# Kernel optimization log

Measured on AMD Instinct MI355X. Metric: run time of the kernel, lower is better.

Reference implementation:

```python
import jax, jax.numpy as jnp
import numpy as np

N = 50000   # nodes
E = 800000  # edges
F = 128     # node_features
H = 128     # hid_channel
G = 128     # graphs in batch


def _lin(k, din, dout):
    s = 1.0 / np.sqrt(din)
    return jax.random.uniform(k, (din, dout), jnp.float32, -s, s)


def setup_inputs() -> dict:
    key = jax.random.key(0)
    ks = jax.random.split(key, 16)
    x = jax.random.normal(ks[0], (N, F), jnp.float32)
    edge_list = jax.random.randint(ks[1], (E, 2), 0, N)
    batch = jnp.sort(jax.random.randint(ks[2], (N,), 0, G))
    inp = {"x": x, "edge_list": edge_list, "batch": batch}
    dims = [(F, H)] + [(H, H)] * 4
    for i, (di, do) in enumerate(dims):
        k1, k2 = jax.random.split(ks[3 + i])
        inp[f"Wl{i+1}"] = _lin(k1, di, do)   # weight on aggregated neighbors
        inp[f"Wr{i+1}"] = _lin(k2, di, do)   # root (self) weight
        inp[f"b{i+1}"] = jnp.zeros((do,), jnp.float32)
    inp["Wf1"] = _lin(ks[10], H, H)
    inp["bf1"] = jnp.zeros((H,), jnp.float32)
    inp["Wf2"] = _lin(ks[11], H, 1)
    inp["bf2"] = jnp.zeros((1,), jnp.float32)
    return inp


def reference(x, edge_list, batch,
              Wl1, Wr1, b1, Wl2, Wr2, b2, Wl3, Wr3, b3,
              Wl4, Wr4, b4, Wl5, Wr5, b5, Wf1, bf1, Wf2, bf2):
    src = edge_list[:, 0]  # message source (x_j)
    dst = edge_list[:, 1]  # aggregation target
    ones_e = jnp.ones((E,), x.dtype)
    deg = jnp.clip(jax.ops.segment_sum(ones_e, dst, num_segments=N), 1.0)

    def sage(h, Wl, Wr, b):
        # scatter-mean of neighbor features, then two linears (PyG SAGEConv, aggr='mean')
        agg = jax.ops.segment_sum(h[src], dst, num_segments=N) / deg[:, None]
        return agg @ Wl + h @ Wr + b

    h = x
    for Wl, Wr, b in ((Wl1, Wr1, b1), (Wl2, Wr2, b2), (Wl3, Wr3, b3),
                      (Wl4, Wr4, b4), (Wl5, Wr5, b5)):
        h = jax.nn.relu(sage(h, Wl, Wr, b))

    # global mean pool over graphs
    cnt = jnp.clip(jax.ops.segment_sum(jnp.ones((N,), h.dtype), batch, num_segments=G), 1.0)
    g = jax.ops.segment_sum(h, batch, num_segments=G) / cnt[:, None]

    g = jax.nn.relu(g @ Wf1 + bf1)
    out = jax.nn.sigmoid(g @ Wf2 + bf2)  # num_classes==1 binary path
    return out.reshape(-1)
```

## Files before the change

### kernel.cpp

```cpp
#include <hip/hip_runtime.h>
#include <math.h>

#define N_NODES 50000
#define MPAD    50048
#define N_EDGES 800000
#define FDIM    128
#define NGRAPH  128

#define NCB   196
#define CBN   256
#define ABLK  256
#define EPB   (N_EDGES / ABLK)
#define CVT_BLOCKS ((MPAD * FDIM / 4 + 255) / 256)

#define NCHUNK 8
#define CHUNK_OF(s) ((int)(((u32)(s) * 671u) >> 22))

typedef __attribute__((ext_vector_type(8))) short short8;
typedef __attribute__((ext_vector_type(4))) float f32x4;
typedef __attribute__((ext_vector_type(2))) float f32x2;
typedef unsigned int u32;

__device__ __forceinline__ unsigned short f2bf(float f) {
    unsigned int u = __float_as_uint(f);
    return (unsigned short)((u + 0x7FFFu + ((u >> 16) & 1u)) >> 16);
}
__device__ __forceinline__ float bfhi(unsigned int u) { return __uint_as_float(u & 0xFFFF0000u); }
__device__ __forceinline__ float bflo(unsigned int u) { return __uint_as_float(u << 16); }

#define ACC16(v) { \
    f32x2 d0 = __builtin_amdgcn_cvt_pk_f32_fp8((int)(v).x, false); \
    f32x2 d1 = __builtin_amdgcn_cvt_pk_f32_fp8((int)(v).x, true);  \
    f32x2 d2 = __builtin_amdgcn_cvt_pk_f32_fp8((int)(v).y, false); \
    f32x2 d3 = __builtin_amdgcn_cvt_pk_f32_fp8((int)(v).y, true);  \
    f32x2 d4 = __builtin_amdgcn_cvt_pk_f32_fp8((int)(v).z, false); \
    f32x2 d5 = __builtin_amdgcn_cvt_pk_f32_fp8((int)(v).z, true);  \
    f32x2 d6 = __builtin_amdgcn_cvt_pk_f32_fp8((int)(v).w, false); \
    f32x2 d7 = __builtin_amdgcn_cvt_pk_f32_fp8((int)(v).w, true);  \
    acc[0] += d0.x;  acc[1] += d0.y;  acc[2] += d1.x;  acc[3] += d1.y; \
    acc[4] += d2.x;  acc[5] += d2.y;  acc[6] += d3.x;  acc[7] += d3.y; \
    acc[8] += d4.x;  acc[9] += d4.y;  acc[10] += d5.x; acc[11] += d5.y; \
    acc[12] += d6.x; acc[13] += d6.y; acc[14] += d7.x; acc[15] += d7.y; }

__global__ __launch_bounds__(256) void pre_kernel(const float* __restrict__ x,
                                                  unsigned short* __restrict__ xb,
                                                  unsigned char* __restrict__ xb8,
                                                  const int* __restrict__ edges,
                                                  int* __restrict__ g_hist) {
    __shared__ int hist[NCB];
    int t = threadIdx.x;
    if (blockIdx.x < CVT_BLOCKS) {
        int i = blockIdx.x * 256 + t;
        if (i >= MPAD * FDIM / 4) return;
        int base = i * 4;
        uint2 o;
        if (base < N_NODES * FDIM) {
            float4 v = *(const float4*)&x[base];
            o.x = (u32)f2bf(v.x) | ((u32)f2bf(v.y) << 16);
            o.y = (u32)f2bf(v.z) | ((u32)f2bf(v.w) << 16);
            int p8 = __builtin_amdgcn_cvt_pk_fp8_f32(v.x, v.y, 0, false);
            p8 = __builtin_amdgcn_cvt_pk_fp8_f32(v.z, v.w, p8, true);
            *(u32*)&xb8[base] = (u32)p8;
        } else { o.x = 0u; o.y = 0u; }
        *(uint2*)&xb[base] = o;
    } else {
        int blk = blockIdx.x - CVT_BLOCKS;
        if (t < NCB) hist[t] = 0;
        __syncthreads();
        int beg = blk * EPB, end = beg + EPB;
        for (int i = beg + t; i < end; i += 256) {
            int2 ed = ((const int2*)edges)[i];
            atomicAdd(&hist[ed.y >> 8], 1);
        }
        __syncthreads();
        if (t < NCB) g_hist[t * ABLK + blk] = hist[t];
    }
}

__global__ __launch_bounds__(64) void scan1_kernel(const int* __restrict__ g_hist,
                                                   int* __restrict__ g_base,
                                                   int* __restrict__ cbtotal) {
    int cbi = blockIdx.x, l = threadIdx.x;
    int4 v = ((const int4*)(g_hist + cbi * ABLK))[l];
    int s1 = v.x + v.y, s2 = s1 + v.z, s3 = s2 + v.w;
    int inc = s3;
    #pragma unroll
    for (int off = 1; off < 64; off <<= 1) {
        int nv = __shfl_up(inc, off, 64);
        if (l >= off) inc += nv;
    }
    int excl = inc - s3;
    int4 o; o.x = excl; o.y = excl + v.x; o.z = excl + s1; o.w = excl + s2;
    ((int4*)(g_base + cbi * ABLK))[l] = o;
    if (l == 63) cbtotal[cbi] = inc;
}

__global__ __launch_bounds__(256) void scan2_kernel(const int* __restrict__ cbtotal,
                                                    int* __restrict__ cbbase,
                                                    int* __restrict__ row_ptr) {
    __shared__ int s[NCB];
    int t = threadIdx.x;
    if (t < NCB) s[t] = cbtotal[t];
    __syncthreads();
    if (t == 0) {
        int run = 0;
        for (int i = 0; i < NCB; ++i) { int v = s[i]; s[i] = run; run += v; }
        row_ptr[N_NODES] = N_EDGES;
    }
    __syncthreads();
    if (t < NCB) cbbase[t] = s[t];
}

__global__ __launch_bounds__(256) void scatter_kernel(const int* __restrict__ edges,
                                                      const int* __restrict__ g_base,
                                                      const int* __restrict__ cbbase,
                                                      u32* __restrict__ coarse) {
    __shared__ int cur[NCB];
    int t = threadIdx.x, blk = blockIdx.x;
    if (t < NCB) cur[t] = g_base[t * ABLK + blk] + cbbase[t];
    __syncthreads();
    int beg = blk * EPB, end = beg + EPB;
    for (int i = beg + t; i < end; i += 256) {
        int2 ed = ((const int2*)edges)[i];
        int cb = ed.y >> 8;
        int pos = atomicAdd(&cur[cb], 1);
        coarse[pos] = ((u32)(ed.y & 255) << 16) | (u32)ed.x;
    }
}

__global__ __launch_bounds__(256) void csr_kernel(const int* __restrict__ cbbase,
                                                  const int* __restrict__ cbtotal,
                                                  const u32* __restrict__ coarse,
                                                  int* __restrict__ csr_src,
                                                  int* __restrict__ row_ptr,
                                                  float* __restrict__ invdeg) {
    __shared__ int cnt[CBN][NCHUNK];
    __shared__ int dbase[CBN];
    int cb = blockIdx.x, t = threadIdx.x;
    int n = cbtotal[cb], base = cbbase[cb];
    #pragma unroll
    for (int c0 = 0; c0 < NCHUNK; ++c0) cnt[t][c0] = 0;
    __syncthreads();
    const u32* ce = coarse + base;
    for (int i = t; i < n; i += 256) {
        u32 ev = ce[i];
        atomicAdd(&cnt[ev >> 16][CHUNK_OF(ev & 0xFFFFu)], 1);
    }
    __syncthreads();
    {
        int run = 0;
        #pragma unroll
        for (int c0 = 0; c0 < NCHUNK; ++c0) { int v = cnt[t][c0]; cnt[t][c0] = run; run += v; }
        dbase[t] = run;
    }
    __syncthreads();
    if (t == 0) {
        int run = base;
        for (int d = 0; d < CBN; ++d) { int v = dbase[d]; dbase[d] = run; run += v; }
    }
    __syncthreads();
    {
        int db = dbase[t];
        int deg = ((t == CBN - 1) ? base + n : dbase[t + 1]) - db;
        #pragma unroll
        for (int c0 = 0; c0 < NCHUNK; ++c0) cnt[t][c0] += db;
        int node = cb * CBN + t;
        if (node < N_NODES) {
            row_ptr[node] = db;
            invdeg[node] = 1.0f / (float)max(deg, 1);
        }
    }
    __syncthreads();
    for (int i = t; i < n; i += 256) {
        u32 ev = ce[i];
        int pos = atomicAdd(&cnt[ev >> 16][CHUNK_OF(ev & 0xFFFFu)], 1);
        csr_src[pos] = (int)(ev & 0xFFFFu);
    }
}

struct WPtrs { const float* wl[5]; const float* wr[5]; };
__global__ void convert_w_kernel(WPtrs wp, unsigned short* __restrict__ wcat,
                                 const int* __restrict__ batch,
                                 float* __restrict__ gsum,
                                 float* __restrict__ invcnt) {
    int t = blockIdx.x * blockDim.x + threadIdx.x;
    if (t < NGRAPH * FDIM) gsum[t] = 0.0f;
    if (t < NGRAPH) {
        int g = t;
        int lo = 0, hi = N_NODES;
        while (lo < hi) { int mid = (lo + hi) >> 1; if (batch[mid] < g) lo = mid + 1; else hi = mid; }
        int beg = lo;
        hi = N_NODES;
        while (lo < hi) { int mid = (lo + hi) >> 1; if (batch[mid] < g + 1) lo = mid + 1; else hi = mid; }
        invcnt[g] = 1.0f / (float)max(lo - beg, 1);
    }
    if (t >= 5 * 128 * 256) return;
    int l = t >> 15;
    int rem = t & 32767;
    int k = rem >> 7;
    int n = rem & 127;
    const float* W = (k < 128) ? wp.wl[l] : wp.wr[l];
    float v = W[(k & 127) * 128 + n];
    wcat[((size_t)l << 15) + n * 256 + k] = f2bf(v);
}

__global__ __launch_bounds__(512) void sage_fused_kernel(
        const unsigned short* __restrict__ h,
        const unsigned char*  __restrict__ h8,
        const int* __restrict__ row_ptr,
        const int* __restrict__ csr_src,
        const float* __restrict__ invdeg,
        const unsigned short* __restrict__ Wcat,
        const float* __restrict__ bias,
        unsigned short* __restrict__ out,
        unsigned char*  __restrict__ out8,
        const int* __restrict__ pool_batch,
        float* __restrict__ gsum) {
    __shared__ unsigned short As[64][136];
    int t = threadIdx.x;
    int node0 = blockIdx.x * 64;

    {
        int slot = t >> 3;
        int lane = t & 7;
        int c = lane * 16;
        int node = node0 + slot;
        float acc[16];
        #pragma unroll
        for (int i = 0; i < 16; ++i) acc[i] = 0.f;
        if (node < N_NODES) {
            int beg = row_ptr[node], end = row_ptr[node + 1];
            int e = beg;
            for (; e + 4 <= end; e += 4) {
                int s0 = csr_src[e + 0];
                int s1 = csr_src[e + 1];
                int s2 = csr_src[e + 2];
                int s3 = csr_src[e + 3];
                uint4 v0 = *(const uint4*)&h8[(size_t)s0 * FDIM + c];
                uint4 v1 = *(const uint4*)&h8[(size_t)s1 * FDIM + c];
                uint4 v2 = *(const uint4*)&h8[(size_t)s2 * FDIM + c];
                uint4 v3 = *(const uint4*)&h8[(size_t)s3 * FDIM + c];
                ACC16(v0); ACC16(v1); ACC16(v2); ACC16(v3);
            }
            for (; e < end; ++e) {
                int s = csr_src[e];
                uint4 v = *(const uint4*)&h8[(size_t)s * FDIM + c];
                ACC16(v);
            }
            float inv = invdeg[node];
            #pragma unroll
            for (int i = 0; i < 16; ++i) acc[i] *= inv;
        }
        uint4 o0, o1;
        o0.x = (u32)f2bf(acc[0])  | ((u32)f2bf(acc[1])  << 16);
        o0.y = (u32)f2bf(acc[2])  | ((u32)f2bf(acc[3])  << 16);
        o0.z = (u32)f2bf(acc[4])  | ((u32)f2bf(acc[5])  << 16);
        o0.w = (u32)f2bf(acc[6])  | ((u32)f2bf(acc[7])  << 16);
        o1.x = (u32)f2bf(acc[8])  | ((u32)f2bf(acc[9])  << 16);
        o1.y = (u32)f2bf(acc[10]) | ((u32)f2bf(acc[11]) << 16);
        o1.z = (u32)f2bf(acc[12]) | ((u32)f2bf(acc[13]) << 16);
        o1.w = (u32)f2bf(acc[14]) | ((u32)f2bf(acc[15]) << 16);
        *(uint4*)&As[slot][c] = o0;
        *(uint4*)&As[slot][c + 8] = o1;
    }
    __syncthreads();

    int wave = t >> 6;
    int lane = t & 63;
    int l15 = lane & 15;
    int q = lane >> 4;
    int stripe = wave >> 1;
    int half = wave & 1;
    int row_base = node0 + stripe * 16;

    f32x4 acc[4];
    #pragma unroll
    for (int i = 0; i < 4; ++i) acc[i] = (f32x4){0.f, 0.f, 0.f, 0.f};

    {
        const unsigned short* Wb = Wcat + (size_t)(half * 64 + l15) * 256 + q * 8;
        #pragma unroll
        for (int k0 = 0; k0 < 128; k0 += 32) {
            short8 a = *(const short8*)&As[stripe * 16 + l15][q * 8 + k0];
            #pragma unroll
            for (int j = 0; j < 4; ++j) {
                short8 b = *(const short8*)(Wb + (size_t)j * 16 * 256 + k0);
                acc[j] = __builtin_amdgcn_mfma_f32_16x16x32_bf16(a, b, acc[j], 0, 0, 0);
            }
        }
    }
    {
        const unsigned short* Ab = h + (size_t)(row_base + l15) * FDIM + q * 8;
        const unsigned short* Wb = Wcat + (size_t)(half * 64 + l15) * 256 + 128 + q * 8;
        #pragma unroll
        for (int k0 = 0; k0 < 128; k0 += 32) {
            short8 a = *(const short8*)(Ab + k0);
            #pragma unroll
            for (int j = 0; j < 4; ++j) {
                short8 b = *(const short8*)(Wb + (size_t)j * 16 * 256 + k0);
                acc[j] = __builtin_amdgcn_mfma_f32_16x16x32_bf16(a, b, acc[j], 0, 0, 0);
            }
        }
    }

    if (pool_batch == nullptr) {
        #pragma unroll
        for (int j = 0; j < 4; ++j) {
            int col = (half * 4 + j) * 16 + l15;
            float bv = bias[col];
            #pragma unroll
            for (int r = 0; r < 4; ++r) {
                int row = row_base + q * 4 + r;
                float v = fmaxf(acc[j][r] + bv, 0.f);
                out[(size_t)row * FDIM + col] = f2bf(v);
                int pk = __builtin_amdgcn_cvt_pk_fp8_f32(v, v, 0, false);
                out8[(size_t)row * FDIM + col] = (unsigned char)(pk & 0xff);
            }
        }
    } else {
        __syncthreads();
        #pragma unroll
        for (int j = 0; j < 4; ++j) {
            int col = (half * 4 + j) * 16 + l15;
            float bv = bias[col];
            #pragma unroll
            for (int r = 0; r < 4; ++r) {
                int rl = stripe * 16 + q * 4 + r;
                As[rl][col] = f2bf(fmaxf(acc[j][r] + bv, 0.f));
            }
        }
        __syncthreads();
        if (t < FDIM) {
            int f = t;
            int nmax = min(64, N_NODES - node0);
            float a = 0.0f;
            int cur = pool_batch[node0];
            for (int r = 0; r < nmax; ++r) {
                int b = pool_batch[node0 + r];
                if (b != cur) {
                    atomicAdd(&gsum[cur * FDIM + f], a);
                    a = 0.0f;
                    cur = b;
                }
                a += bflo((u32)As[r][f]);
            }
            atomicAdd(&gsum[cur * FDIM + f], a);
        }
    }
}

__global__ void mlp_kernel(const float* __restrict__ gsum,
                           const float* __restrict__ invcnt,
                           const float* __restrict__ Wf1, const float* __restrict__ bf1,
                           const float* __restrict__ Wf2, const float* __restrict__ bf2,
                           float* __restrict__ out) {
    int gg = blockIdx.x;
    int j = threadIdx.x;
    __shared__ float row[128];
    __shared__ float red[128];
    row[j] = gsum[gg * 128 + j] * invcnt[gg];
    __syncthreads();
    float acc = bf1[j];
    for (int k = 0; k < 128; ++k) acc = fmaf(row[k], Wf1[k * 128 + j], acc);
    float v = fmaxf(acc, 0.0f);
    red[j] = v * Wf2[j];
    __syncthreads();
    for (int off = 64; off > 0; off >>= 1) {
        if (j < off) red[j] += red[j + off];
        __syncthreads();
    }
    if (j == 0) out[gg] = 1.0f / (1.0f + expf(-(red[0] + bf2[0])));
}

extern "C" void kernel_launch(void* const* d_in, const int* in_sizes, int n_in,
                              void* d_out, int out_size, void* d_ws, size_t ws_size,
                              hipStream_t stream) {
    const float* x      = (const float*)d_in[0];
    const int*   edges  = (const int*)d_in[1];
    const int*   batch  = (const int*)d_in[2];
    WPtrs wp;
    const float* bs[5];
    for (int l = 0; l < 5; ++l) {
        wp.wl[l] = (const float*)d_in[3 + 3 * l];
        wp.wr[l] = (const float*)d_in[4 + 3 * l];
        bs[l]    = (const float*)d_in[5 + 3 * l];
    }
    const float* Wf1 = (const float*)d_in[18];
    const float* bf1 = (const float*)d_in[19];
    const float* Wf2 = (const float*)d_in[20];
    const float* bf2 = (const float*)d_in[21];
    float* out = (float*)d_out;

    char* ws = (char*)d_ws;
    auto alloc = [&](size_t bytes) { void* p = (void*)ws; ws += (bytes + 255) & ~(size_t)255; return p; };
    unsigned short* xb   = (unsigned short*)alloc((size_t)MPAD * FDIM * 2);
    unsigned short* hA   = (unsigned short*)alloc((size_t)MPAD * FDIM * 2);
    unsigned short* hB   = (unsigned short*)alloc((size_t)MPAD * FDIM * 2);
    unsigned short* wcat = (unsigned short*)alloc((size_t)5 * 128 * 256 * 2);
    u32*   coarse   = (u32*)alloc((size_t)N_EDGES * 4);
    int*   g_hist   = (int*)alloc((size_t)NCB * ABLK * 4);
    int*   g_base   = (int*)alloc((size_t)NCB * ABLK * 4);
    int*   cbbase   = (int*)alloc((size_t)NCB * 4);
    int*   cbtotal  = (int*)alloc((size_t)NCB * 4);
    int*   row_ptr  = (int*)alloc((size_t)(N_NODES + 1) * 4);
    int*   csr_src  = (int*)alloc((size_t)N_EDGES * 4);
    float* invdeg   = (float*)alloc((size_t)N_NODES * 4);
    float* gsum     = (float*)alloc((size_t)NGRAPH * FDIM * 4);
    float* invcnt   = (float*)alloc((size_t)NGRAPH * 4);
    unsigned char* h8A = (unsigned char*)alloc((size_t)MPAD * FDIM);
    unsigned char* xb8 = (unsigned char*)hB;
    unsigned char* h8B = (unsigned char*)xb;
    (void)ws_size; (void)in_sizes; (void)n_in; (void)out_size;

    pre_kernel<<<CVT_BLOCKS + ABLK, 256, 0, stream>>>(x, xb, xb8, edges, g_hist);
    convert_w_kernel<<<(5 * 128 * 256 + 255) / 256, 256, 0, stream>>>(wp, wcat, batch, gsum, invcnt);
    scan1_kernel<<<NCB, 64, 0, stream>>>(g_hist, g_base, cbtotal);
    scan2_kernel<<<1, 256, 0, stream>>>(cbtotal, cbbase, row_ptr);
    scatter_kernel<<<ABLK, 256, 0, stream>>>(edges, g_base, cbbase, coarse);
    csr_kernel<<<NCB, 256, 0, stream>>>(cbbase, cbtotal, coarse, csr_src, row_ptr, invdeg);

    const unsigned short* hcur  = xb;
    const unsigned char*  h8cur = xb8;
    unsigned short* bufs[2]  = {hA, hB};
    unsigned char*  bufs8[2] = {h8A, h8B};
    for (int l = 0; l < 5; ++l) {
        unsigned short* hnext  = bufs[l & 1];
        unsigned char*  h8next = (l == 4) ? nullptr : bufs8[l & 1];
        const int* pb = (l == 4) ? batch : nullptr;
        sage_fused_kernel<<<MPAD / 64, 512, 0, stream>>>(
            hcur, h8cur, row_ptr, csr_src, invdeg, wcat + ((size_t)l << 15), bs[l],
            hnext, h8next, pb, gsum);
        hcur = hnext;
        h8cur = bufs8[l & 1];
    }

    mlp_kernel<<<NGRAPH, 128, 0, stream>>>(gsum, invcnt, Wf1, bf1, Wf2, bf2, out);
}
```

Baseline: 424.2 us.

## Merge setup kernels, fuse scans via last-block pattern, and shrink SAGE tiles

Folds the weight conversion, pooling-count and gsum zeroing work into pre_kernel as extra blocks, and merges the two scan kernels into one by having the last finishing block compute the coarse-bucket prefix through an atomic counter. It also halves the sage_fused_kernel tile from 64 to 32 nodes per block, with 256 threads instead of 512. The aim is fewer kernel launches and better occupancy or load balance in the main layers. The cost is serial work in one thread of the last scan block, plus any part of the sage kernel body not visible here that may still assume 512 threads and 64 rows.

```diff
diff --git a/kernel.cpp b/kernel.cpp
--- a/kernel.cpp
+++ b/kernel.cpp
@@ -12,6 +12,7 @@
 #define ABLK  256
 #define EPB   (N_EDGES / ABLK)
 #define CVT_BLOCKS ((MPAD * FDIM / 4 + 255) / 256)
+#define WCONV_BLOCKS 640
 
 #define NCHUNK 8
 #define CHUNK_OF(s) ((int)(((u32)(s) * 671u) >> 22))
@@ -42,13 +43,22 @@
     acc[8] += d4.x;  acc[9] += d4.y;  acc[10] += d5.x; acc[11] += d5.y; \
     acc[12] += d6.x; acc[13] += d6.y; acc[14] += d7.x; acc[15] += d7.y; }
 
+struct WPtrs { const float* wl[5]; const float* wr[5]; };
+
 __global__ __launch_bounds__(256) void pre_kernel(const float* __restrict__ x,
                                                   unsigned short* __restrict__ xb,
                                                   unsigned char* __restrict__ xb8,
                                                   const int* __restrict__ edges,
-                                                  int* __restrict__ g_hist) {
+                                                  int* __restrict__ g_hist,
+                                                  WPtrs wp,
+                                                  unsigned short* __restrict__ wcat,
+                                                  const int* __restrict__ batch,
+                                                  float* __restrict__ gsum,
+                                                  float* __restrict__ invcnt,
+                                                  int* __restrict__ done) {
     __shared__ int hist[NCB];
     int t = threadIdx.x;
+    if (blockIdx.x == 0 && t == 0) *done = 0;
     if (blockIdx.x < CVT_BLOCKS) {
         int i = blockIdx.x * 256 + t;
         if (i >= MPAD * FDIM / 4) return;
@@ -63,7 +73,7 @@
             *(u32*)&xb8[base] = (u32)p8;
         } else { o.x = 0u; o.y = 0u; }
         *(uint2*)&xb[base] = o;
-    } else {
+    } else if (blockIdx.x < CVT_BLOCKS + ABLK) {
         int blk = blockIdx.x - CVT_BLOCKS;
         if (t < NCB) hist[t] = 0;
         __syncthreads();
@@ -74,12 +84,34 @@
         }
         __syncthreads();
         if (t < NCB) g_hist[t * ABLK + blk] = hist[t];
-    }
-}
-
-__global__ __launch_bounds__(64) void scan1_kernel(const int* __restrict__ g_hist,
-                                                   int* __restrict__ g_base,
-                                                   int* __restrict__ cbtotal) {
+    } else {
+        int tg = (blockIdx.x - CVT_BLOCKS - ABLK) * 256 + t;
+        if (tg < NGRAPH * FDIM) gsum[tg] = 0.0f;
+        if (tg < NGRAPH) {
+            int g = tg;
+            int lo = 0, hi = N_NODES;
+            while (lo < hi) { int mid = (lo + hi) >> 1; if (batch[mid] < g) lo = mid + 1; else hi = mid; }
+            int beg = lo;
+            hi = N_NODES;
+            while (lo < hi) { int mid = (lo + hi) >> 1; if (batch[mid] < g + 1) lo = mid + 1; else hi = mid; }
+            invcnt[g] = 1.0f / (float)max(lo - beg, 1);
+        }
+        int l = tg >> 15;
+        int rem = tg & 32767;
+        int k = rem >> 7;
+        int n = rem & 127;
+        const float* W = (k < 128) ? wp.wl[l] : wp.wr[l];
+        float v = W[(k & 127) * 128 + n];
+        wcat[((size_t)l << 15) + n * 256 + k] = f2bf(v);
+    }
+}
+
+__global__ __launch_bounds__(64) void scan_kernel(const int* __restrict__ g_hist,
+                                                  int* __restrict__ g_base,
+                                                  int* __restrict__ cbtotal,
+                                                  int* __restrict__ cbbase,
+                                                  int* __restrict__ row_ptr,
+                                                  int* __restrict__ done) {
     int cbi = blockIdx.x, l = threadIdx.x;
     int4 v = ((const int4*)(g_hist + cbi * ABLK))[l];
     int s1 = v.x + v.y, s2 = s1 + v.z, s3 = s2 + v.w;
@@ -92,23 +124,19 @@
     int excl = inc - s3;
     int4 o; o.x = excl; o.y = excl + v.x; o.z = excl + s1; o.w = excl + s2;
     ((int4*)(g_base + cbi * ABLK))[l] = o;
-    if (l == 63) cbtotal[cbi] = inc;
-}
-
-__global__ __launch_bounds__(256) void scan2_kernel(const int* __restrict__ cbtotal,
-                                                    int* __restrict__ cbbase,
-                                                    int* __restrict__ row_ptr) {
-    __shared__ int s[NCB];
-    int t = threadIdx.x;
-    if (t < NCB) s[t] = cbtotal[t];
-    __syncthreads();
-    if (t == 0) {
+    if (l == 63) atomicExch(&cbtotal[cbi], inc);
+    __threadfence();
+    int last = 0;
+    if (l == 0) last = (atomicAdd(done, 1) == NCB - 1) ? 1 : 0;
+    last = __shfl(last, 0, 64);
+    if (last && l == 0) {
         int run = 0;
-        for (int i = 0; i < NCB; ++i) { int v = s[i]; s[i] = run; run += v; }
+        for (int i = 0; i < NCB; ++i) {
+            int ti = atomicAdd(&cbtotal[i], 0);
+            cbbase[i] = run; run += ti;
+        }
         row_ptr[N_NODES] = N_EDGES;
     }
-    __syncthreads();
-    if (t < NCB) cbbase[t] = s[t];
 }
 
 __global__ __launch_bounds__(256) void scatter_kernel(const int* __restrict__ edges,
@@ -178,33 +206,7 @@
     }
 }
 
-struct WPtrs { const float* wl[5]; const float* wr[5]; };
-__global__ void convert_w_kernel(WPtrs wp, unsigned short* __restrict__ wcat,
-                                 const int* __restrict__ batch,
-                                 float* __restrict__ gsum,
-                                 float* __restrict__ invcnt) {
-    int t = blockIdx.x * blockDim.x + threadIdx.x;
-    if (t < NGRAPH * FDIM) gsum[t] = 0.0f;
-    if (t < NGRAPH) {
-        int g = t;
-        int lo = 0, hi = N_NODES;
-        while (lo < hi) { int mid = (lo + hi) >> 1; if (batch[mid] < g) lo = mid + 1; else hi = mid; }
-        int beg = lo;
-        hi = N_NODES;
-        while (lo < hi) { int mid = (lo + hi) >> 1; if (batch[mid] < g + 1) lo = mid + 1; else hi = mid; }
-        invcnt[g] = 1.0f / (float)max(lo - beg, 1);
-    }
-    if (t >= 5 * 128 * 256) return;
-    int l = t >> 15;
-    int rem = t & 32767;
-    int k = rem >> 7;
-    int n = rem & 127;
-    const float* W = (k < 128) ? wp.wl[l] : wp.wr[l];
-    float v = W[(k & 127) * 128 + n];
-    wcat[((size_t)l << 15) + n * 256 + k] = f2bf(v);
-}
-
-__global__ __launch_bounds__(512) void sage_fused_kernel(
+__global__ __launch_bounds__(256) void sage_fused_kernel(
         const unsigned short* __restrict__ h,
         const unsigned char*  __restrict__ h8,
         const int* __restrict__ row_ptr,
@@ -216,9 +218,9 @@
         unsigned char*  __restrict__ out8,
         const int* __restrict__ pool_batch,
         float* __restrict__ gsum) {
-    __shared__ unsigned short As[64][136];
+    __shared__ unsigned short As[32][136];
     int t = threadIdx.x;
-    int node0 = blockIdx.x * 64;
+    int node0 = blockIdx.x * 32;
 
     {
         int slot = t >> 3;
@@ -332,7 +334,7 @@
         __syncthreads();
         if (t < FDIM) {
             int f = t;
-            int nmax = min(64, N_NODES - node0);
+            int nmax = min(32, N_NODES - node0);
             float a = 0.0f;
             int cur = pool_batch[node0];
             for (int r = 0; r < nmax; ++r) {
@@ -407,15 +409,15 @@
     float* invdeg   = (float*)alloc((size_t)N_NODES * 4);
     float* gsum     = (float*)alloc((size_t)NGRAPH * FDIM * 4);
     float* invcnt   = (float*)alloc((size_t)NGRAPH * 4);
+    int*   done     = (int*)alloc(256);
     unsigned char* h8A = (unsigned char*)alloc((size_t)MPAD * FDIM);
     unsigned char* xb8 = (unsigned char*)hB;
     unsigned char* h8B = (unsigned char*)xb;
     (void)ws_size; (void)in_sizes; (void)n_in; (void)out_size;
 
-    pre_kernel<<<CVT_BLOCKS + ABLK, 256, 0, stream>>>(x, xb, xb8, edges, g_hist);
-    convert_w_kernel<<<(5 * 128 * 256 + 255) / 256, 256, 0, stream>>>(wp, wcat, batch, gsum, invcnt);
-    scan1_kernel<<<NCB, 64, 0, stream>>>(g_hist, g_base, cbtotal);
-    scan2_kernel<<<1, 256, 0, stream>>>(cbtotal, cbbase, row_ptr);
+    pre_kernel<<<CVT_BLOCKS + ABLK + WCONV_BLOCKS, 256, 0, stream>>>(
+        x, xb, xb8, edges, g_hist, wp, wcat, batch, gsum, invcnt, done);
+    scan_kernel<<<NCB, 64, 0, stream>>>(g_hist, g_base, cbtotal, cbbase, row_ptr, done);
     scatter_kernel<<<ABLK, 256, 0, stream>>>(edges, g_base, cbbase, coarse);
     csr_kernel<<<NCB, 256, 0, stream>>>(cbbase, cbtotal, coarse, csr_src, row_ptr, invdeg);
 
@@ -427,7 +429,7 @@
         unsigned short* hnext  = bufs[l & 1];
         unsigned char*  h8next = (l == 4) ? nullptr : bufs8[l & 1];
         const int* pb = (l == 4) ? batch : nullptr;
-        sage_fused_kernel<<<MPAD / 64, 512, 0, stream>>>(
+        sage_fused_kernel<<<MPAD / 32, 256, 0, stream>>>(
             hcur, h8cur, row_ptr, csr_src, invdeg, wcat + ((size_t)l << 15), bs[l],
             hnext, h8next, pb, gsum);
         hcur = hnext;
```

Result: faster. 414.8 us (-2.2%).
